# Kernel optimization log

Hardware: AMD Instinct MI355X
Metric: run time of the kernel (lower is better)

Reference implementation:

```python
import jax, jax.numpy as jnp
import numpy as np

B, S, E, HID, NTR, NCAL, CW, VOCAB, POS = 4096, 201, 32, 512, 4, 8, 16, 32, 256
LN_EPS = 1e-5


def _ln(x, g, b):
    m = x.mean(-1, keepdims=True)
    v = ((x - m) ** 2).mean(-1, keepdims=True)
    return (x - m) * jax.lax.rsqrt(v + LN_EPS) * g + b


def setup_inputs() -> dict:
    key = jax.random.key(0)
    ks = jax.random.split(key, 24)
    g = lambda i, shape, s=0.1: (jax.random.normal(ks[i], shape, jnp.float32) * s)
    return dict(
        encoded_seq=jax.random.randint(ks[0], (B, S), 0, VOCAB, jnp.int32),
        experiment_id=jax.random.randint(ks[1], (B,), 0, NCAL, jnp.int32),
        tok_emb=g(2, (VOCAB, E), 1.0),
        pos_emb=g(3, (POS, E), 1.0),
        ln1_g=jnp.ones((NTR, E)), ln1_b=jnp.zeros((NTR, E)),
        wq=g(4, (NTR, E, E)), wk=g(5, (NTR, E, E)), wv=g(6, (NTR, E, E)),
        bq=g(7, (NTR, E), 0.01), bk=g(8, (NTR, E), 0.01), bv=g(9, (NTR, E), 0.01),
        wo=g(10, (NTR, E, E)), bo=g(11, (NTR, E), 0.01),
        ln2_g=jnp.ones((NTR, E)), ln2_b=jnp.zeros((NTR, E)),
        w1=g(12, (NTR, E, HID)), b1=g(13, (NTR, HID), 0.01),
        w2=g(14, (NTR, HID, E)), b2=g(15, (NTR, E), 0.01),
        lnf_g=jnp.ones((E,)), lnf_b=jnp.zeros((E,)),
        wpen=g(16, (E, 1)), bpen=g(17, (1,), 0.01),
        wfan=g(18, (1, CW)), bfan=g(19, (CW,), 0.01),
        wcal=g(20, (NCAL, CW, 1)), bcal=g(21, (NCAL, 1), 0.01),
    )


def reference(encoded_seq, experiment_id, tok_emb, pos_emb,
              ln1_g, ln1_b, wq, wk, wv, bq, bk, bv, wo, bo,
              ln2_g, ln2_b, w1, b1, w2, b2,
              lnf_g, lnf_b, wpen, bpen, wfan, bfan, wcal, bcal):
    # embedding + positional add: [B,S,E]
    x = tok_emb[encoded_seq] + pos_emb[jnp.arange(S)]
    scale = 1.0 / jnp.sqrt(jnp.float32(E))  # num_heads=1 => head_dim=E
    for i in range(NTR):
        n = _ln(x, ln1_g[i], ln1_b[i])
        q = n @ wq[i] + bq[i]
        k = n @ wk[i] + bk[i]
        v = n @ wv[i] + bv[i]
        a = jax.nn.softmax(jnp.einsum('bqe,bke->bqk', q, k) * scale, axis=-1)
        att = jnp.einsum('bqk,bke->bqe', a, v) @ wo[i] + bo[i]
        x = x + att
        h = _ln(x, ln2_g[i], ln2_b[i])
        x = x + (jax.nn.silu(h @ w1[i] + b1[i]) @ w2[i] + b2[i])
    contrib = _ln(x, lnf_g, lnf_b) @ wpen + bpen        # [B,S,1]
    underlying = contrib.sum(axis=-2)                    # [B,1]
    pre = jax.nn.elu(underlying @ wfan + bfan)           # [B,CW]
    # all calibrator heads at once: [B,NCAL]
    all_corr = jnp.einsum('bc,ncj->bn', pre, wcal) + bcal[:, 0]
    mask = jax.nn.one_hot(experiment_id, NCAL, dtype=pre.dtype)  # exactly the (exp==id) mask-sum
    corrected = (all_corr * mask).sum(-1, keepdims=True) + underlying
    return corrected.squeeze()
```

## Files before the change

kernel.cpp:

```cpp
#include <hip/hip_runtime.h>


#define SS   201
#define SP   208
#define NMT  13
#define EE   32
#define HIDN 512
#define NTRL 4
#define CWN  16
#define BB   4096
#define XST  36
#define QST  36
#define MST  72
#define VWST 228

#define X_OFF    0
#define K_OFF    14976
#define VWT_OFF  29952
#define QS_OFF   44544
#define MS_OFF   49152
#define RS_OFF   49984
#define BIAS_OFF 50816
#define SMEM_SZ  51840

#define WS_FRAG  0
#define WS_BIAS  294912
#define WS_B1    299008
#define WS_FIN   307200
#define L2E      1.4426950408889634f

typedef unsigned short u16;
typedef unsigned int   u32;
typedef short bf16x4 __attribute__((ext_vector_type(4)));
typedef short bf16x8 __attribute__((ext_vector_type(8)));
typedef float f32x4  __attribute__((ext_vector_type(4)));
typedef float f32x2  __attribute__((ext_vector_type(2)));

#define CBAR asm volatile("" ::: "memory")

__device__ __forceinline__ f32x4 MF(bf16x8 a, bf16x8 b, f32x4 c){
  return __builtin_amdgcn_mfma_f32_16x16x32_bf16(a, b, c, 0, 0, 0);
}
__device__ __forceinline__ float bf2f(u16 u){ return __uint_as_float(((u32)u)<<16); }
__device__ __forceinline__ u16 f2bf(float f){
  u32 u = __float_as_uint(f);
  u += 0x7fffu + ((u>>16)&1u);
  return (u16)(u>>16);
}
__device__ __forceinline__ u16 f2bf_fast(float f){
  return (u16)((__float_as_uint(f) + 0x8000u) >> 16);
}
__device__ __forceinline__ u32 pk2bf(f32x2 v){
#if defined(__has_builtin) && __has_builtin(__builtin_amdgcn_cvt_pk_bf16_f32)
  auto r = __builtin_amdgcn_cvt_pk_bf16_f32(v.x, v.y);
  u32 u; __builtin_memcpy(&u, &r, 4); return u;
#else
  return ((__float_as_uint(v.x)+0x8000u)>>16) | ((__float_as_uint(v.y)+0x8000u) & 0xffff0000u);
#endif
}
template<bool F32>
__device__ __forceinline__ float ldv(const void* p, int i){
  if (F32) return ((const float*)p)[i];
  return bf2f(((const u16*)p)[i]);
}
template<bool F32>
__device__ __forceinline__ u16 ldbf(const void* p, int i){
  if (F32) return f2bf(((const float*)p)[i]);
  return ((const u16*)p)[i];
}
__device__ __forceinline__ bf16x8 ld8(const u16* p){
  const bf16x4* q = (const bf16x4*)p;
  bf16x4 lo = q[0], hi = q[1];
  bf16x8 r = {lo[0],lo[1],lo[2],lo[3],hi[0],hi[1],hi[2],hi[3]};
  return r;
}

__device__ __forceinline__ int sniff_bf16(const void* tok_emb, int tid){
  int sane = 0;
  if (tid < 64){
    u16 wd = ((const u16*)tok_emb)[tid];
    int e = (wd >> 7) & 0xFF;
    sane = (e >= 100 && e <= 140) ? 1 : 0;
  }
  return (__syncthreads_count(sane) >= 52) ? 1 : 0;
}

template<bool F32>
__device__ __forceinline__ void frag_body(const void* wq, const void* wk,
    const void* wv, const void* wo, const void* w1, const void* w2, void* ws)
{
  int t = blockIdx.x;
  int l = t / 72, k = t % 72;
  int lane = threadIdx.x, l16 = lane & 15, quad = lane >> 4;
  bf16x8 v;
  if (k < 8){
    int mat = k >> 1, half = k & 1;
    const void* src = (mat==0)? wq : (mat==1)? wk : (mat==2)? wv : wo;
    #pragma unroll
    for (int j=0;j<8;j++)
      v[j] = (short)ldbf<F32>(src, l*1024 + (quad*8+j)*32 + half*16 + l16);
  } else if (k < 40){
    int nt = k - 8;
    #pragma unroll
    for (int j=0;j<8;j++)
      v[j] = (short)ldbf<F32>(w1, l*16384 + (quad*8+j)*512 + nt*16 + l16);
  } else {
    int kc = (k-40)>>1, nh = (k-40)&1;
    #pragma unroll
    for (int j=0;j<8;j++)
      v[j] = (short)ldbf<F32>(w2, l*16384 + (kc*32+quad*8+j)*32 + nh*16 + l16);
  }
  *(bf16x8*)((char*)ws + WS_FRAG + t*1024 + lane*16) = v;
}

__global__ __launch_bounds__(64) void fmt_frags(
    const void* __restrict__ tok_emb,
    const void* __restrict__ wq, const void* __restrict__ wk,
    const void* __restrict__ wv, const void* __restrict__ wo,
    const void* __restrict__ w1, const void* __restrict__ w2,
    void* __restrict__ ws)
{
  if (sniff_bf16(tok_emb, threadIdx.x)) frag_body<false>(wq,wk,wv,wo,w1,w2,ws);
  else                                  frag_body<true >(wq,wk,wv,wo,w1,w2,ws);
}

template<bool F32>
__device__ __forceinline__ void bias_body(
    const void* bq, const void* bk, const void* bv, const void* wo, const void* bo,
    const void* ln1_g, const void* ln1_b, const void* ln2_g, const void* ln2_b,
    const void* b1, const void* b2,
    const void* lnf_g, const void* lnf_b, const void* wpen, const void* bpen,
    const void* wfan, const void* bfan, const void* wcal, const void* bcal,
    void* ws)
{
  int tid = threadIdx.x, idx = tid & 31, grp = tid >> 5;
  float* BW  = (float*)((char*)ws + WS_BIAS);
  float* BW1 = (float*)((char*)ws + WS_B1);
  float* FW  = (float*)((char*)ws + WS_FIN);
  for (int l=0;l<NTRL;l++){
    float v = 0.f;
    switch(grp){
      case 0: v = ldv<F32>(bq, l*32+idx); break;
      case 1: v = ldv<F32>(bk, l*32+idx); break;
      case 2: {
        float acc = ldv<F32>(bo, l*32+idx);
        for (int e=0;e<EE;e++) acc += ldv<F32>(bv, l*32+e) * ldv<F32>(wo, l*1024 + e*32 + idx);
        v = acc; break;
      }
      case 3: v = ldv<F32>(ln1_g, l*32+idx); break;
      case 4: v = ldv<F32>(ln1_b, l*32+idx); break;
      case 5: v = ldv<F32>(ln2_g, l*32+idx); break;
      case 6: v = ldv<F32>(ln2_b, l*32+idx); break;
      case 7: v = ldv<F32>(b2,   l*32+idx); break;
    }
    BW[l*256 + tid] = v;
  }
  for (int i=tid; i<NTRL*HIDN; i+=256) BW1[i] = ldv<F32>(b1, i);
  if (tid < 32){
    FW[tid]    = ldv<F32>(lnf_g, tid);
    FW[32+tid] = ldv<F32>(lnf_b, tid);
    FW[64+tid] = ldv<F32>(wpen, tid);
  }
  if (tid == 0) FW[96] = ldv<F32>(bpen, 0);
  if (tid < 16){ FW[97+tid] = ldv<F32>(wfan, tid); FW[113+tid] = ldv<F32>(bfan, tid); }
  if (tid < 128) FW[129+tid] = ldv<F32>(wcal, tid);
  if (tid < 8)   FW[257+tid] = ldv<F32>(bcal, tid);
}

__global__ __launch_bounds__(256) void fmt_bias(
    const void* __restrict__ tok_emb,
    const void* __restrict__ bq, const void* __restrict__ bk,
    const void* __restrict__ bv, const void* __restrict__ wo, const void* __restrict__ bo,
    const void* __restrict__ ln1_g, const void* __restrict__ ln1_b,
    const void* __restrict__ ln2_g, const void* __restrict__ ln2_b,
    const void* __restrict__ b1, const void* __restrict__ b2,
    const void* __restrict__ lnf_g, const void* __restrict__ lnf_b,
    const void* __restrict__ wpen, const void* __restrict__ bpen,
    const void* __restrict__ wfan, const void* __restrict__ bfan,
    const void* __restrict__ wcal, const void* __restrict__ bcal,
    void* __restrict__ ws)
{
  if (sniff_bf16(tok_emb, threadIdx.x))
    bias_body<false>(bq,bk,bv,wo,bo,ln1_g,ln1_b,ln2_g,ln2_b,b1,b2,
                     lnf_g,lnf_b,wpen,bpen,wfan,bfan,wcal,bcal,ws);
  else
    bias_body<true >(bq,bk,bv,wo,bo,ln1_g,ln1_b,ln2_g,ln2_b,b1,b2,
                     lnf_g,lnf_b,wpen,bpen,wfan,bfan,wcal,bcal,ws);
}

__device__ __forceinline__ void ln_stats(const u16* Xb, float* MS, float* RS, int tid){
  if (tid < SP){
    const u32* row = (const u32*)(Xb + tid*XST);
    f32x2 v[16]; f32x2 s2 = {0.f,0.f};
    #pragma unroll
    for (int i=0;i<16;i++){
      u32 d = row[i];
      f32x2 p = { __uint_as_float(d<<16), __uint_as_float(d & 0xffff0000u) };
      v[i] = p; s2 += p;
    }
    float m = (s2.x + s2.y) * (1.f/EE);
    f32x2 m2 = {m, m};
    f32x2 var2 = {0.f,0.f};
    #pragma unroll
    for (int i=0;i<16;i++){ f32x2 d = v[i]-m2; var2 += d*d; }
    MS[tid] = m;
    RS[tid] = rsqrtf((var2.x+var2.y)*(1.f/EE) + 1e-5f);
  }
}

__device__ __forceinline__ bf16x8 build_nfrag(const u16* Xb, const float* MS, const float* RS,
                                              int row, int quad, const f32x2* G2, const f32x2* B2){
  const u32* raw = (const u32*)(Xb + row*XST + quad*8);
  f32x2 m2 = { MS[row], MS[row] };
  f32x2 rs2 = { RS[row], RS[row] };
  u32 o[4];
  #pragma unroll
  for (int p=0;p<4;p++){
    u32 d = raw[p];
    f32x2 x = { __uint_as_float(d<<16), __uint_as_float(d & 0xffff0000u) };
    f32x2 t = (x - m2) * rs2;
    f32x2 v = t * G2[p] + B2[p];
    o[p] = pk2bf(v);
  }
  bf16x8 r; __builtin_memcpy(&r, o, 16);
  return r;
}

template<bool F32>
__device__ __forceinline__ void tr_body(
    const int* seq, const int* expid,
    const void* tok_emb, const void* pos_emb,
    const void* ws, void* out, unsigned char* smem)
{
  u16*   Xb   = (u16*)(smem + X_OFF);
  u16*   Kb   = (u16*)(smem + K_OFF);
  u16*   VWTb = (u16*)(smem + VWT_OFF);
  u16*   QSb  = (u16*)(smem + QS_OFF);
  float* MS   = (float*)(smem + MS_OFF);
  float* RS   = (float*)(smem + RS_OFF);
  float* BIAS = (float*)(smem + BIAS_OFF);

  const int tid  = threadIdx.x;
  const int lane = tid & 63, w = tid >> 6;
  const int l16  = lane & 15, quad = lane >> 4;
  const int b    = blockIdx.x;
  const f32x4 Z  = {0.f,0.f,0.f,0.f};
  u16* qs = QSb + w*576;
  u16* qm = (u16*)(smem + VWT_OFF) + w*1152;

  {
    const int* srow = seq + b*SS;
    for (int i = tid; i < SP*EE; i += 256){
      int s = i >> 5, e = i & 31;
      float val = 0.f;
      if (s < SS){
        int tok = srow[s];
        val = ldv<F32>(tok_emb, tok*EE + e) + ldv<F32>(pos_emb, s*EE + e);
      }
      Xb[s*XST + e] = f2bf(val);
    }
  }
  __syncthreads();

  const float qce = 0.2550546813f;
  const f32x2 qce2 = {qce, qce};
  const f32x2 one2 = {1.f, 1.f};
  const f32x2 nl2e2 = {-L2E, -L2E};

  for (int l = 0; l < NTRL; ++l){
    const char* wsl = (const char*)ws + WS_FRAG + l*73728;
    bf16x8 bwq0 = *(const bf16x8*)(wsl + 0*1024 + lane*16);
    bf16x8 bwq1 = *(const bf16x8*)(wsl + 1*1024 + lane*16);
    bf16x8 bwk0 = *(const bf16x8*)(wsl + 2*1024 + lane*16);
    bf16x8 bwk1 = *(const bf16x8*)(wsl + 3*1024 + lane*16);
    bf16x8 bwv0 = *(const bf16x8*)(wsl + 4*1024 + lane*16);
    bf16x8 bwv1 = *(const bf16x8*)(wsl + 5*1024 + lane*16);
    bf16x8 bwo0 = *(const bf16x8*)(wsl + 6*1024 + lane*16);
    bf16x8 bwo1 = *(const bf16x8*)(wsl + 7*1024 + lane*16);
    {
      const float* BW = (const float*)((const char*)ws + WS_BIAS) + l*256;
      BIAS[tid] = BW[tid];
    }
    for (int i = tid; i < 32*16; i += 256)
      VWTb[(i>>4)*VWST + 208 + (i&15)] = 0;
    ln_stats(Xb, MS, RS, tid);
    __syncthreads();

    bf16x8 aq[4];
    {
      f32x2 G2[4], B2[4];
      #pragma unroll
      for (int p=0;p<4;p++){
        G2[p] = f32x2{BIAS[96+quad*8+2*p], BIAS[96+quad*8+2*p+1]};
        B2[p] = f32x2{BIAS[128+quad*8+2*p], BIAS[128+quad*8+2*p+1]};
      }
      f32x2 bqb2 = {BIAS[l16],    BIAS[16+l16]};
      f32x2 bkb2 = {BIAS[32+l16], BIAS[48+l16]};
      #pragma unroll
      for (int t=0;t<4;t++){
        int m = w + 4*t;
        if (m < NMT){
          int m16 = m*16;
          bf16x8 an = build_nfrag(Xb, MS, RS, m16+l16, quad, G2, B2);
          f32x4 ck0 = MF(an, bwk0, Z), ck1 = MF(an, bwk1, Z);
          #pragma unroll
          for (int r=0;r<4;r++){
            int row = m16 + quad*4 + r;
            u32 pk = pk2bf(f32x2{ck0[r], ck1[r]} + bkb2);
            Kb[row*XST + l16]      = (u16)pk;
            Kb[row*XST + 16 + l16] = (u16)(pk>>16);
          }
          f32x4 cq0 = MF(an, bwq0, Z), cq1 = MF(an, bwq1, Z);
          #pragma unroll
          for (int r=0;r<4;r++){
            u32 pk = pk2bf((f32x2{cq0[r], cq1[r]} + bqb2) * qce2);
            qs[(quad*4+r)*QST + l16]      = (u16)pk;
            qs[(quad*4+r)*QST + 16 + l16] = (u16)(pk>>16);
          }
          CBAR;
          aq[t] = ld8(qs + l16*QST + quad*8);
          CBAR;
          f32x4 cv0 = MF(an, bwv0, Z), cv1 = MF(an, bwv1, Z);
          #pragma unroll
          for (int r=0;r<4;r++){
            u32 pk = pk2bf(f32x2{cv0[r], cv1[r]});
            qs[(quad*4+r)*QST + l16]      = (u16)pk;
            qs[(quad*4+r)*QST + 16 + l16] = (u16)(pk>>16);
          }
          CBAR;
          bf16x8 av = ld8(qs + l16*QST + quad*8);
          CBAR;
          f32x4 cw0 = MF(av, bwo0, Z), cw1 = MF(av, bwo1, Z);
          #pragma unroll
          for (int r=0;r<4;r++){
            u32 pk = pk2bf(f32x2{cw0[r], cw1[r]});
            VWTb[l16*VWST      + m16 + quad*4 + r] = (u16)pk;
            VWTb[(16+l16)*VWST + m16 + quad*4 + r] = (u16)(pk>>16);
          }
        }
      }
    }
    __syncthreads();

    {
      f32x2 OB2 = {BIAS[64+l16], BIAS[80+l16]};
      #pragma unroll
      for (int t=0;t<4;t++){
        int m = w + 4*t;
        if (m < NMT){
          int m16 = m*16;
          f32x4 S[13];
          #pragma unroll
          for (int j=0;j<13;j++){
            bf16x8 kb8 = ld8(Kb + (j*16+l16)*XST + quad*8);
            S[j] = MF(aq[t], kb8, Z);
          }
          f32x2 sa = {0.f,0.f}, sb = {0.f,0.f};
          #pragma unroll
          for (int j=0;j<13;j++){
            float e0 = __builtin_amdgcn_exp2f(S[j][0]);
            float e1 = __builtin_amdgcn_exp2f(S[j][1]);
            float e2 = __builtin_amdgcn_exp2f(S[j][2]);
            float e3 = __builtin_amdgcn_exp2f(S[j][3]);
            if (j==12 && l16 >= 9){ e0=0.f; e1=0.f; e2=0.f; e3=0.f; }
            S[j] = f32x4{e0,e1,e2,e3};
            sa += f32x2{e0,e1}; sb += f32x2{e2,e3};
          }
          float sm[4] = {sa.x, sa.y, sb.x, sb.y};
          #pragma unroll
          for (int d=1; d<16; d<<=1){
            #pragma unroll
            for (int r=0;r<4;r++) sm[r] += __shfl_xor(sm[r], d);
          }
          float inv[4];
          #pragma unroll
          for (int r=0;r<4;r++) inv[r] = __builtin_amdgcn_rcpf(sm[r]);

          f32x4 o0 = Z, o1 = Z;
          #pragma unroll
          for (int c=0;c<7;c++){
            #pragma unroll
            for (int jj=0;jj<2;jj++){
              int j = 2*c + jj;
              u32 pk0 = 0, pk1 = 0;
              if (j < 13){
                pk0 = pk2bf(f32x2{S[j][0], S[j][1]});
                pk1 = pk2bf(f32x2{S[j][2], S[j][3]});
              }
              qs[(quad*4+0)*QST + jj*16 + l16] = (u16)pk0;
              qs[(quad*4+1)*QST + jj*16 + l16] = (u16)(pk0>>16);
              qs[(quad*4+2)*QST + jj*16 + l16] = (u16)pk1;
              qs[(quad*4+3)*QST + jj*16 + l16] = (u16)(pk1>>16);
            }
            CBAR;
            bf16x8 ap = ld8(qs + l16*QST + quad*8);
            bf16x8 b0 = ld8(VWTb + l16*VWST      + c*32 + quad*8);
            bf16x8 b1f = ld8(VWTb + (16+l16)*VWST + c*32 + quad*8);
            o0 = MF(ap, b0, o0); o1 = MF(ap, b1f, o1);
            CBAR;
          }
          #pragma unroll
          for (int r=0;r<4;r++){
            int row = m16 + quad*4 + r;
            u16* x0 = Xb + row*XST + l16;
            u16* x1 = Xb + row*XST + 16 + l16;
            f32x2 xv = { bf2f(*x0), bf2f(*x1) };
            f32x2 iv = { inv[r], inv[r] };
            f32x2 ov = f32x2{o0[r], o1[r]} * iv + (xv + OB2);
            u32 pk = pk2bf(ov);
            *x0 = (u16)pk; *x1 = (u16)(pk>>16);
          }
        }
      }
    }
    __syncthreads();

    ln_stats(Xb, MS, RS, tid);
    __syncthreads();

    {
      f32x2 G2[4], B2[4];
      #pragma unroll
      for (int p=0;p<4;p++){
        G2[p] = f32x2{BIAS[160+quad*8+2*p], BIAS[160+quad*8+2*p+1]};
        B2[p] = f32x2{BIAS[192+quad*8+2*p], BIAS[192+quad*8+2*p+1]};
      }
      bf16x8 anc[4];
      #pragma unroll
      for (int t=0;t<4;t++){
        int m = w + 4*t;
        if (m < NMT) anc[t] = build_nfrag(Xb, MS, RS, m*16+l16, quad, G2, B2);
      }
      f32x4 oacc[4][2];
      #pragma unroll
      for (int t=0;t<4;t++){ oacc[t][0] = Z; oacc[t][1] = Z; }
      const char* w1f = wsl + 8*1024;
      const char* w2f = wsl + 40*1024;
      const float* BW1 = (const float*)((const char*)ws + WS_B1) + l*HIDN;

      for (int hc = 0; hc < HIDN; hc += 64){
        bf16x8 bw1[4], bw2[2][2];
        #pragma unroll
        for (int nt=0;nt<4;nt++)
          bw1[nt] = *(const bf16x8*)(w1f + (hc/16 + nt)*1024 + lane*16);
        #pragma unroll
        for (int kc=0;kc<2;kc++){
          bw2[kc][0] = *(const bf16x8*)(w2f + ((hc/32 + kc)*2    )*1024 + lane*16);
          bw2[kc][1] = *(const bf16x8*)(w2f + ((hc/32 + kc)*2 + 1)*1024 + lane*16);
        }
        f32x2 b1v2[4];
        #pragma unroll
        for (int nt=0;nt<4;nt++){
          float bb = BW1[hc + nt*16 + l16];
          b1v2[nt] = f32x2{bb, bb};
        }
        #pragma unroll
        for (int t=0;t<4;t++){
          int m = w + 4*t;
          if (m < NMT){
            #pragma unroll
            for (int nt=0;nt<4;nt++){
              f32x4 h = MF(anc[t], bw1[nt], Z);
              #pragma unroll
              for (int rp=0;rp<2;rp++){
                f32x2 z = f32x2{h[2*rp], h[2*rp+1]} + b1v2[nt];
                f32x2 a = z * nl2e2;
                f32x2 e = { __builtin_amdgcn_exp2f(a.x), __builtin_amdgcn_exp2f(a.y) };
                f32x2 d = one2 + e;
                f32x2 rc = { __builtin_amdgcn_rcpf(d.x), __builtin_amdgcn_rcpf(d.y) };
                f32x2 s = z * rc;
                u32 pk = pk2bf(s);
                qm[(quad*4+2*rp  )*MST + nt*16 + l16] = (u16)pk;
                qm[(quad*4+2*rp+1)*MST + nt*16 + l16] = (u16)(pk>>16);
              }
            }
            CBAR;
            bf16x8 ah0 = ld8(qm + l16*MST + quad*8);
            bf16x8 ah1 = ld8(qm + l16*MST + 32 + quad*8);
            oacc[t][0] = MF(ah0, bw2[0][0], oacc[t][0]);
            oacc[t][0] = MF(ah1, bw2[1][0], oacc[t][0]);
            oacc[t][1] = MF(ah0, bw2[0][1], oacc[t][1]);
            oacc[t][1] = MF(ah1, bw2[1][1], oacc[t][1]);
            CBAR;
          }
        }
      }

      f32x2 b2v2 = {BIAS[224+l16], BIAS[240+l16]};
      #pragma unroll
      for (int t=0;t<4;t++){
        int m = w + 4*t;
        if (m < NMT){
          int m16 = m*16;
          #pragma unroll
          for (int r=0;r<4;r++){
            int row = m16 + quad*4 + r;
            u16* x0 = Xb + row*XST + l16;
            u16* x1 = Xb + row*XST + 16 + l16;
            f32x2 xv = { bf2f(*x0), bf2f(*x1) };
            f32x2 ov = f32x2{oacc[t][0][r], oacc[t][1][r]} + (xv + b2v2);
            u32 pk = pk2bf(ov);
            *x0 = (u16)pk; *x1 = (u16)(pk>>16);
          }
        }
      }
    }
    __syncthreads();
  }

  const float* FW = (const float*)((const char*)ws + WS_FIN);
  if (tid < 32){
    BIAS[tid]    = FW[tid];
    BIAS[32+tid] = FW[32+tid];
    BIAS[64+tid] = FW[64+tid];
  }
  __syncthreads();
  float part = 0.f;
  if (tid < SS){
    const u32* row = (const u32*)(Xb + tid*XST);
    f32x2 v[16]; f32x2 s2 = {0.f,0.f};
    #pragma unroll
    for (int i=0;i<16;i++){
      u32 d = row[i];
      f32x2 p = { __uint_as_float(d<<16), __uint_as_float(d & 0xffff0000u) };
      v[i] = p; s2 += p;
    }
    float m = (s2.x+s2.y) * (1.f/EE);
    f32x2 m2 = {m,m};
    f32x2 var2 = {0.f,0.f};
    #pragma unroll
    for (int i=0;i<16;i++){ f32x2 d = v[i]-m2; var2 += d*d; }
    float rs = rsqrtf((var2.x+var2.y)*(1.f/EE) + 1e-5f);
    f32x2 rs2 = {rs, rs};
    f32x2 dot2 = {0.f,0.f};
    #pragma unroll
    for (int i=0;i<16;i++){
      f32x2 g = {BIAS[2*i], BIAS[2*i+1]};
      f32x2 bb = {BIAS[32+2*i], BIAS[33+2*i]};
      f32x2 wp = {BIAS[64+2*i], BIAS[65+2*i]};
      f32x2 n = (v[i]-m2)*rs2*g + bb;
      dot2 += n*wp;
    }
    part = dot2.x + dot2.y + FW[96];
  }
  #pragma unroll
  for (int off=32; off; off>>=1) part += __shfl_xor(part, off);
  float* REDF = (float*)(smem + QS_OFF);
  __syncthreads();
  if (lane == 0) REDF[w] = part;
  __syncthreads();
  if (tid == 0){
    float u = REDF[0] + REDF[1] + REDF[2] + REDF[3];
    int ex = expid[b];
    float corr = FW[257+ex];
    #pragma unroll
    for (int c = 0; c < CWN; ++c){
      float pre = u * FW[97+c] + FW[113+c];
      pre = pre > 0.f ? pre : (__expf(pre) - 1.f);
      corr += pre * FW[129 + ex*CWN + c];
    }
    float res = corr + u;
    if (F32) ((float*)out)[b] = res;
    else     ((u16*)out)[b]  = f2bf(res);
  }
}

__global__ __launch_bounds__(256, 3) void tr_kernel(
    const int* __restrict__ seq, const int* __restrict__ expid,
    const void* __restrict__ tok_emb, const void* __restrict__ pos_emb,
    const void* __restrict__ ws, void* __restrict__ out)
{
  __shared__ __align__(16) unsigned char smem[SMEM_SZ];
  if (sniff_bf16(tok_emb, threadIdx.x))
    tr_body<false>(seq, expid, tok_emb, pos_emb, ws, out, smem);
  else
    tr_body<true >(seq, expid, tok_emb, pos_emb, ws, out, smem);
}

extern "C" void kernel_launch(void* const* d_in, const int* in_sizes, int n_in,
                              void* d_out, int out_size, void* d_ws, size_t ws_size,
                              hipStream_t stream)
{
  (void)in_sizes; (void)n_in; (void)ws_size; (void)out_size;
  const void* tok_emb = d_in[2];
  fmt_frags<<<dim3(288), dim3(64), 0, stream>>>(
      tok_emb, d_in[6], d_in[7], d_in[8], d_in[12], d_in[16], d_in[18], d_ws);
  fmt_bias<<<dim3(1), dim3(256), 0, stream>>>(
      tok_emb, d_in[9], d_in[10], d_in[11], d_in[12], d_in[13],
      d_in[4], d_in[5], d_in[14], d_in[15], d_in[17], d_in[19],
      d_in[20], d_in[21], d_in[22], d_in[23],
      d_in[24], d_in[25], d_in[26], d_in[27], d_ws);
  tr_kernel<<<dim3(BB), dim3(256), 0, stream>>>(
      (const int*)d_in[0], (const int*)d_in[1], tok_emb, d_in[3], d_ws, d_out);
}
```

Baseline: 1.002 ms.

## Fold Wv·Wo into one weight, interleave columns, double-buffer the MLP SiLU scratch

The weight-prep kernel now precomputes the product Wv·Wo per layer. The main kernel then projects the normalized input straight to the V·Wo result and drops one MFMA stage, its LDS round trip and two wave barriers per tile. Fragment columns are interleaved (even/odd) so each lane writes packed u32 pairs of bf16 for K, Q, the residual updates and the SiLU activations, instead of separate u16 stores. The MLP loop now ping-pongs between two SiLU scratch buffers placed in the K region, which is free at that point. This lets the next tile's W1/SiLU be computed before the current W2 MFMA and removes the CBARs. The cost is extra rounding from the bf16 fused Wv·Wo weight and reliance on in-wave LDS ordering without explicit barriers.

```diff
diff --git a/kernel.cpp b/kernel.cpp
--- a/kernel.cpp
+++ b/kernel.cpp
@@ -58,6 +58,9 @@
   return ((__float_as_uint(v.x)+0x8000u)>>16) | ((__float_as_uint(v.y)+0x8000u) & 0xffff0000u);
 #endif
 }
+__device__ __forceinline__ f32x2 upk2(u32 d){
+  return f32x2{ __uint_as_float(d<<16), __uint_as_float(d & 0xffff0000u) };
+}
 template<bool F32>
 __device__ __forceinline__ float ldv(const void* p, int i){
   if (F32) return ((const float*)p)[i];
@@ -93,22 +96,36 @@
   int l = t / 72, k = t % 72;
   int lane = threadIdx.x, l16 = lane & 15, quad = lane >> 4;
   bf16x8 v;
-  if (k < 8){
-    int mat = k >> 1, half = k & 1;
-    const void* src = (mat==0)? wq : (mat==1)? wk : (mat==2)? wv : wo;
+  if (k < 2){
     #pragma unroll
     for (int j=0;j<8;j++)
-      v[j] = (short)ldbf<F32>(src, l*1024 + (quad*8+j)*32 + half*16 + l16);
-  } else if (k < 40){
-    int nt = k - 8;
+      v[j] = (short)ldbf<F32>(wq, l*1024 + (quad*8+j)*32 + 2*l16 + k);
+  } else if (k < 4){
     #pragma unroll
     for (int j=0;j<8;j++)
-      v[j] = (short)ldbf<F32>(w1, l*16384 + (quad*8+j)*512 + nt*16 + l16);
+      v[j] = (short)ldbf<F32>(wk, l*1024 + (quad*8+j)*32 + 2*l16 + (k-2));
+  } else if (k < 6){
+    int col = 2*l16 + (k-4);
+    #pragma unroll
+    for (int j=0;j<8;j++){
+      int a = quad*8 + j;
+      float acc = 0.f;
+      for (int e=0;e<EE;e++)
+        acc += ldv<F32>(wv, l*1024 + a*32 + e) * ldv<F32>(wo, l*1024 + e*32 + col);
+      v[j] = (short)f2bf(acc);
+    }
+  } else if (k < 38){
+    int g = (k-6)>>1, par = (k-6)&1;
+    #pragma unroll
+    for (int j=0;j<8;j++)
+      v[j] = (short)ldbf<F32>(w1, l*16384 + (quad*8+j)*512 + g*32 + 2*l16 + par);
+  } else if (k < 70){
+    int kc = (k-38)>>1, par = (k-38)&1;
+    #pragma unroll
+    for (int j=0;j<8;j++)
+      v[j] = (short)ldbf<F32>(w2, l*16384 + (kc*32+quad*8+j)*32 + 2*l16 + par);
   } else {
-    int kc = (k-40)>>1, nh = (k-40)&1;
-    #pragma unroll
-    for (int j=0;j<8;j++)
-      v[j] = (short)ldbf<F32>(w2, l*16384 + (kc*32+quad*8+j)*32 + nh*16 + l16);
+    v = bf16x8{0,0,0,0,0,0,0,0};
   }
   *(bf16x8*)((char*)ws + WS_FRAG + t*1024 + lane*16) = v;
 }
@@ -193,11 +210,7 @@
     const u32* row = (const u32*)(Xb + tid*XST);
     f32x2 v[16]; f32x2 s2 = {0.f,0.f};
     #pragma unroll
-    for (int i=0;i<16;i++){
-      u32 d = row[i];
-      f32x2 p = { __uint_as_float(d<<16), __uint_as_float(d & 0xffff0000u) };
-      v[i] = p; s2 += p;
-    }
+    for (int i=0;i<16;i++){ f32x2 p = upk2(row[i]); v[i] = p; s2 += p; }
     float m = (s2.x + s2.y) * (1.f/EE);
     f32x2 m2 = {m, m};
     f32x2 var2 = {0.f,0.f};
@@ -216,11 +229,8 @@
   u32 o[4];
   #pragma unroll
   for (int p=0;p<4;p++){
-    u32 d = raw[p];
-    f32x2 x = { __uint_as_float(d<<16), __uint_as_float(d & 0xffff0000u) };
-    f32x2 t = (x - m2) * rs2;
-    f32x2 v = t * G2[p] + B2[p];
-    o[p] = pk2bf(v);
+    f32x2 x = upk2(raw[p]);
+    o[p] = pk2bf((x - m2) * rs2 * G2[p] + B2[p]);
   }
   bf16x8 r; __builtin_memcpy(&r, o, 16);
   return r;
@@ -245,8 +255,9 @@
   const int l16  = lane & 15, quad = lane >> 4;
   const int b    = blockIdx.x;
   const f32x4 Z  = {0.f,0.f,0.f,0.f};
-  u16* qs = QSb + w*576;
-  u16* qm = (u16*)(smem + VWT_OFF) + w*1152;
+  u16* qs  = QSb + w*576;
+  u16* qm0 = (u16*)(smem + K_OFF) + w*2304;
+  u16* qm1 = qm0 + 1152;
 
   {
     const int* srow = seq + b*SS;
@@ -275,8 +286,6 @@
     bf16x8 bwk1 = *(const bf16x8*)(wsl + 3*1024 + lane*16);
     bf16x8 bwv0 = *(const bf16x8*)(wsl + 4*1024 + lane*16);
     bf16x8 bwv1 = *(const bf16x8*)(wsl + 5*1024 + lane*16);
-    bf16x8 bwo0 = *(const bf16x8*)(wsl + 6*1024 + lane*16);
-    bf16x8 bwo1 = *(const bf16x8*)(wsl + 7*1024 + lane*16);
     {
       const float* BW = (const float*)((const char*)ws + WS_BIAS) + l*256;
       BIAS[tid] = BW[tid];
@@ -291,11 +300,11 @@
       f32x2 G2[4], B2[4];
       #pragma unroll
       for (int p=0;p<4;p++){
-        G2[p] = f32x2{BIAS[96+quad*8+2*p], BIAS[96+quad*8+2*p+1]};
-        B2[p] = f32x2{BIAS[128+quad*8+2*p], BIAS[128+quad*8+2*p+1]};
-      }
-      f32x2 bqb2 = {BIAS[l16],    BIAS[16+l16]};
-      f32x2 bkb2 = {BIAS[32+l16], BIAS[48+l16]};
+        G2[p] = *(const f32x2*)(BIAS + 96 + quad*8 + 2*p);
+        B2[p] = *(const f32x2*)(BIAS + 128 + quad*8 + 2*p);
+      }
+      f32x2 bqp = *(const f32x2*)(BIAS + 2*l16);
+      f32x2 bkp = *(const f32x2*)(BIAS + 32 + 2*l16);
       #pragma unroll
       for (int t=0;t<4;t++){
         int m = w + 4*t;
@@ -304,46 +313,28 @@
           bf16x8 an = build_nfrag(Xb, MS, RS, m16+l16, quad, G2, B2);
           f32x4 ck0 = MF(an, bwk0, Z), ck1 = MF(an, bwk1, Z);
           #pragma unroll
+          for (int r=0;r<4;r++)
+            ((u32*)(Kb + (m16+quad*4+r)*XST))[l16] = pk2bf(f32x2{ck0[r], ck1[r]} + bkp);
+          f32x4 cq0 = MF(an, bwq0, Z), cq1 = MF(an, bwq1, Z);
+          #pragma unroll
+          for (int r=0;r<4;r++)
+            ((u32*)(qs + (quad*4+r)*QST))[l16] = pk2bf((f32x2{cq0[r], cq1[r]} + bqp)*qce2);
+          f32x4 cw0 = MF(an, bwv0, Z), cw1 = MF(an, bwv1, Z);
+          #pragma unroll
           for (int r=0;r<4;r++){
-            int row = m16 + quad*4 + r;
-            u32 pk = pk2bf(f32x2{ck0[r], ck1[r]} + bkb2);
-            Kb[row*XST + l16]      = (u16)pk;
-            Kb[row*XST + 16 + l16] = (u16)(pk>>16);
-          }
-          f32x4 cq0 = MF(an, bwq0, Z), cq1 = MF(an, bwq1, Z);
-          #pragma unroll
-          for (int r=0;r<4;r++){
-            u32 pk = pk2bf((f32x2{cq0[r], cq1[r]} + bqb2) * qce2);
-            qs[(quad*4+r)*QST + l16]      = (u16)pk;
-            qs[(quad*4+r)*QST + 16 + l16] = (u16)(pk>>16);
+            VWTb[(2*l16  )*VWST + m16 + quad*4 + r] = f2bf_fast(cw0[r]);
+            VWTb[(2*l16+1)*VWST + m16 + quad*4 + r] = f2bf_fast(cw1[r]);
           }
           CBAR;
           aq[t] = ld8(qs + l16*QST + quad*8);
           CBAR;
-          f32x4 cv0 = MF(an, bwv0, Z), cv1 = MF(an, bwv1, Z);
-          #pragma unroll
-          for (int r=0;r<4;r++){
-            u32 pk = pk2bf(f32x2{cv0[r], cv1[r]});
-            qs[(quad*4+r)*QST + l16]      = (u16)pk;
-            qs[(quad*4+r)*QST + 16 + l16] = (u16)(pk>>16);
-          }
-          CBAR;
-          bf16x8 av = ld8(qs + l16*QST + quad*8);
-          CBAR;
-          f32x4 cw0 = MF(av, bwo0, Z), cw1 = MF(av, bwo1, Z);
-          #pragma unroll
-          for (int r=0;r<4;r++){
-            u32 pk = pk2bf(f32x2{cw0[r], cw1[r]});
-            VWTb[l16*VWST      + m16 + quad*4 + r] = (u16)pk;
-            VWTb[(16+l16)*VWST + m16 + quad*4 + r] = (u16)(pk>>16);
-          }
         }
       }
     }
     __syncthreads();
 
     {
-      f32x2 OB2 = {BIAS[64+l16], BIAS[80+l16]};
+      f32x2 OB2 = *(const f32x2*)(BIAS + 64 + 2*l16);
       #pragma unroll
       for (int t=0;t<4;t++){
         int m = w + 4*t;
@@ -393,22 +384,18 @@
               qs[(quad*4+3)*QST + jj*16 + l16] = (u16)(pk1>>16);
             }
             CBAR;
-            bf16x8 ap = ld8(qs + l16*QST + quad*8);
-            bf16x8 b0 = ld8(VWTb + l16*VWST      + c*32 + quad*8);
-            bf16x8 b1f = ld8(VWTb + (16+l16)*VWST + c*32 + quad*8);
+            bf16x8 ap  = ld8(qs + l16*QST + quad*8);
+            bf16x8 b0  = ld8(VWTb + (2*l16  )*VWST + c*32 + quad*8);
+            bf16x8 b1f = ld8(VWTb + (2*l16+1)*VWST + c*32 + quad*8);
             o0 = MF(ap, b0, o0); o1 = MF(ap, b1f, o1);
             CBAR;
           }
           #pragma unroll
           for (int r=0;r<4;r++){
-            int row = m16 + quad*4 + r;
-            u16* x0 = Xb + row*XST + l16;
-            u16* x1 = Xb + row*XST + 16 + l16;
-            f32x2 xv = { bf2f(*x0), bf2f(*x1) };
+            u32* xp = (u32*)(Xb + (m16+quad*4+r)*XST) + l16;
+            f32x2 xv = upk2(*xp);
             f32x2 iv = { inv[r], inv[r] };
-            f32x2 ov = f32x2{o0[r], o1[r]} * iv + (xv + OB2);
-            u32 pk = pk2bf(ov);
-            *x0 = (u16)pk; *x1 = (u16)(pk>>16);
+            *xp = pk2bf(f32x2{o0[r], o1[r]} * iv + (xv + OB2));
           }
         }
       }
@@ -422,8 +409,8 @@
       f32x2 G2[4], B2[4];
       #pragma unroll
       for (int p=0;p<4;p++){
-        G2[p] = f32x2{BIAS[160+quad*8+2*p], BIAS[160+quad*8+2*p+1]};
-        B2[p] = f32x2{BIAS[192+quad*8+2*p], BIAS[192+quad*8+2*p+1]};
+        G2[p] = *(const f32x2*)(BIAS + 160 + quad*8 + 2*p);
+        B2[p] = *(const f32x2*)(BIAS + 192 + quad*8 + 2*p);
       }
       bf16x8 anc[4];
       #pragma unroll
@@ -434,59 +421,63 @@
       f32x4 oacc[4][2];
       #pragma unroll
       for (int t=0;t<4;t++){ oacc[t][0] = Z; oacc[t][1] = Z; }
-      const char* w1f = wsl + 8*1024;
-      const char* w2f = wsl + 40*1024;
       const float* BW1 = (const float*)((const char*)ws + WS_B1) + l*HIDN;
 
-      for (int hc = 0; hc < HIDN; hc += 64){
-        bf16x8 bw1[4], bw2[2][2];
-        #pragma unroll
-        for (int nt=0;nt<4;nt++)
-          bw1[nt] = *(const bf16x8*)(w1f + (hc/16 + nt)*1024 + lane*16);
-        #pragma unroll
-        for (int kc=0;kc<2;kc++){
-          bw2[kc][0] = *(const bf16x8*)(w2f + ((hc/32 + kc)*2    )*1024 + lane*16);
-          bw2[kc][1] = *(const bf16x8*)(w2f + ((hc/32 + kc)*2 + 1)*1024 + lane*16);
-        }
-        f32x2 b1v2[4];
-        #pragma unroll
-        for (int nt=0;nt<4;nt++){
-          float bb = BW1[hc + nt*16 + l16];
-          b1v2[nt] = f32x2{bb, bb};
-        }
+      for (int c = 0; c < 8; ++c){
+        const char* f1 = wsl + (6 + 4*c)*1024;
+        const char* f2 = wsl + (38 + 4*c)*1024;
+        bf16x8 w1e0 = *(const bf16x8*)(f1 + 0*1024 + lane*16);
+        bf16x8 w1o0 = *(const bf16x8*)(f1 + 1*1024 + lane*16);
+        bf16x8 w1e1 = *(const bf16x8*)(f1 + 2*1024 + lane*16);
+        bf16x8 w1o1 = *(const bf16x8*)(f1 + 3*1024 + lane*16);
+        bf16x8 w2e0 = *(const bf16x8*)(f2 + 0*1024 + lane*16);
+        bf16x8 w2o0 = *(const bf16x8*)(f2 + 1*1024 + lane*16);
+        bf16x8 w2e1 = *(const bf16x8*)(f2 + 2*1024 + lane*16);
+        bf16x8 w2o1 = *(const bf16x8*)(f2 + 3*1024 + lane*16);
+        int hc = c*64;
+        f32x2 b1p0 = *(const f32x2*)(BW1 + hc + 2*l16);
+        f32x2 b1p1 = *(const f32x2*)(BW1 + hc + 32 + 2*l16);
+
+        auto silu_t = [&](int t, u16* dst){
+          f32x4 he0 = MF(anc[t], w1e0, Z), ho0 = MF(anc[t], w1o0, Z);
+          f32x4 he1 = MF(anc[t], w1e1, Z), ho1 = MF(anc[t], w1o1, Z);
+          #pragma unroll
+          for (int r=0;r<4;r++){
+            u32* drow = (u32*)(dst + (quad*4+r)*MST);
+            f32x2 z0 = f32x2{he0[r], ho0[r]} + b1p0;
+            f32x2 a0 = z0 * nl2e2;
+            f32x2 e0 = { __builtin_amdgcn_exp2f(a0.x), __builtin_amdgcn_exp2f(a0.y) };
+            f32x2 d0 = one2 + e0;
+            f32x2 rc0 = { __builtin_amdgcn_rcpf(d0.x), __builtin_amdgcn_rcpf(d0.y) };
+            drow[l16] = pk2bf(z0 * rc0);
+            f32x2 z1 = f32x2{he1[r], ho1[r]} + b1p1;
+            f32x2 a1 = z1 * nl2e2;
+            f32x2 e1 = { __builtin_amdgcn_exp2f(a1.x), __builtin_amdgcn_exp2f(a1.y) };
+            f32x2 d1 = one2 + e1;
+            f32x2 rc1 = { __builtin_amdgcn_rcpf(d1.x), __builtin_amdgcn_rcpf(d1.y) };
+            drow[16 + l16] = pk2bf(z1 * rc1);
+          }
+        };
+
+        silu_t(0, qm0);
         #pragma unroll
         for (int t=0;t<4;t++){
           int m = w + 4*t;
           if (m < NMT){
-            #pragma unroll
-            for (int nt=0;nt<4;nt++){
-              f32x4 h = MF(anc[t], bw1[nt], Z);
-              #pragma unroll
-              for (int rp=0;rp<2;rp++){
-                f32x2 z = f32x2{h[2*rp], h[2*rp+1]} + b1v2[nt];
-                f32x2 a = z * nl2e2;
-                f32x2 e = { __builtin_amdgcn_exp2f(a.x), __builtin_amdgcn_exp2f(a.y) };
-                f32x2 d = one2 + e;
-                f32x2 rc = { __builtin_amdgcn_rcpf(d.x), __builtin_amdgcn_rcpf(d.y) };
-                f32x2 s = z * rc;
-                u32 pk = pk2bf(s);
-                qm[(quad*4+2*rp  )*MST + nt*16 + l16] = (u16)pk;
-                qm[(quad*4+2*rp+1)*MST + nt*16 + l16] = (u16)(pk>>16);
-              }
-            }
-            CBAR;
-            bf16x8 ah0 = ld8(qm + l16*MST + quad*8);
-            bf16x8 ah1 = ld8(qm + l16*MST + 32 + quad*8);
-            oacc[t][0] = MF(ah0, bw2[0][0], oacc[t][0]);
-            oacc[t][0] = MF(ah1, bw2[1][0], oacc[t][0]);
-            oacc[t][1] = MF(ah0, bw2[0][1], oacc[t][1]);
-            oacc[t][1] = MF(ah1, bw2[1][1], oacc[t][1]);
-            CBAR;
+            if (t < 3 && (w + 4*(t+1)) < NMT)
+              silu_t(t+1, (t&1) ? qm0 : qm1);
+            u16* src = (t&1) ? qm1 : qm0;
+            bf16x8 ah0 = ld8(src + l16*MST + quad*8);
+            bf16x8 ah1 = ld8(src + l16*MST + 32 + quad*8);
+            oacc[t][0] = MF(ah0, w2e0, oacc[t][0]);
+            oacc[t][0] = MF(ah1, w2e1, oacc[t][0]);
+            oacc[t][1] = MF(ah0, w2o0, oacc[t][1]);
+            oacc[t][1] = MF(ah1, w2o1, oacc[t][1]);
           }
         }
       }
 
-      f32x2 b2v2 = {BIAS[224+l16], BIAS[240+l16]};
+      f32x2 b2p = *(const f32x2*)(BIAS + 224 + 2*l16);
       #pragma unroll
       for (int t=0;t<4;t++){
         int m = w + 4*t;
@@ -494,13 +485,9 @@
           int m16 = m*16;
           #pragma unroll
           for (int r=0;r<4;r++){
-            int row = m16 + quad*4 + r;
-            u16* x0 = Xb + row*XST + l16;
-            u16* x1 = Xb + row*XST + 16 + l16;
-            f32x2 xv = { bf2f(*x0), bf2f(*x1) };
-            f32x2 ov = f32x2{oacc[t][0][r], oacc[t][1][r]} + (xv + b2v2);
-            u32 pk = pk2bf(ov);
-            *x0 = (u16)pk; *x1 = (u16)(pk>>16);
+            u32* xp = (u32*)(Xb + (m16+quad*4+r)*XST) + l16;
+            f32x2 xv = upk2(*xp);
+            *xp = pk2bf(f32x2{oacc[t][0][r], oacc[t][1][r]} + (xv + b2p));
           }
         }
       }
@@ -520,11 +507,7 @@
     const u32* row = (const u32*)(Xb + tid*XST);
     f32x2 v[16]; f32x2 s2 = {0.f,0.f};
     #pragma unroll
-    for (int i=0;i<16;i++){
-      u32 d = row[i];
-      f32x2 p = { __uint_as_float(d<<16), __uint_as_float(d & 0xffff0000u) };
-      v[i] = p; s2 += p;
-    }
+    for (int i=0;i<16;i++){ f32x2 p = upk2(row[i]); v[i] = p; s2 += p; }
     float m = (s2.x+s2.y) * (1.f/EE);
     f32x2 m2 = {m,m};
     f32x2 var2 = {0.f,0.f};
@@ -535,11 +518,10 @@
     f32x2 dot2 = {0.f,0.f};
     #pragma unroll
     for (int i=0;i<16;i++){
-      f32x2 g = {BIAS[2*i], BIAS[2*i+1]};
-      f32x2 bb = {BIAS[32+2*i], BIAS[33+2*i]};
-      f32x2 wp = {BIAS[64+2*i], BIAS[65+2*i]};
-      f32x2 n = (v[i]-m2)*rs2*g + bb;
-      dot2 += n*wp;
+      f32x2 g  = *(const f32x2*)(BIAS + 2*i);
+      f32x2 bb = *(const f32x2*)(BIAS + 32 + 2*i);
+      f32x2 wp = *(const f32x2*)(BIAS + 64 + 2*i);
+      dot2 += ((v[i]-m2)*rs2*g + bb) * wp;
     }
     part = dot2.x + dot2.y + FW[96];
   }
```

Result: slower. 1.251 ms (+24.8%).
